# Performance work log

Measured on AMD Instinct MI355X. Metric: run time of the kernel, lower is better.

Reference implementation:

```python
import jax, jax.numpy as jnp
import numpy as np

N = 100000      # num POIs (nodes)
M = 20000       # num trajectories (hyperedges)
NNZ = 1000000   # incidence entries
D = 128         # emb_dim
NUM_LAYERS = 3
NEG_SLOPE = 0.2  # PyG HypergraphConv leaky_relu default


def setup_inputs() -> dict:
    key = jax.random.key(0)
    ks = jax.random.split(key, 8)
    pois_embs = jax.random.normal(ks[0], (N, D), jnp.float32)
    traj_embs = jax.random.normal(ks[1], (M, D), jnp.float32)
    hyperedge_weight = jax.random.uniform(ks[2], (M,), jnp.float32)
    node_idx = jax.random.randint(ks[3], (NNZ,), 0, N, jnp.int32)
    edge_idx = jax.random.randint(ks[4], (NNZ,), 0, M, jnp.int32)
    # learned params of the shared HypergraphConv layer (heads=1, concat)
    W_lin = jax.random.normal(ks[5], (D, D), jnp.float32) / np.sqrt(D).astype(np.float32)
    att = jax.random.normal(ks[6], (2 * D,), jnp.float32) * 0.1
    bias = jnp.zeros((D,), jnp.float32)
    return dict(pois_embs=pois_embs, traj_embs=traj_embs,
                hyperedge_weight=hyperedge_weight,
                node_idx=node_idx, edge_idx=edge_idx,
                W_lin=W_lin, att=att, bias=bias)


def _segment_softmax(scores, seg, num_seg):
    smax = jax.ops.segment_max(scores, seg, num_segments=num_seg)
    smax = jnp.where(jnp.isfinite(smax), smax, 0.0)  # guard empty segments
    ex = jnp.exp(scores - smax[seg])
    den = jax.ops.segment_sum(ex, seg, num_segments=num_seg)
    return ex / (den[seg] + 1e-16)


def _hconv(x, traj_embs, hyperedge_weight, node_idx, edge_idx, W_lin, att, bias):
    # x: [N, D] node feats; traj_embs: [M, D] hyperedge feats
    xt = x @ W_lin            # [N, D]  lin(x)
    et = traj_embs @ W_lin    # [M, D]  lin(hyperedge_attr)
    # attention logits per incidence pair (additive decomposition of cat*att)
    s_n = xt @ att[:D]        # [N]
    s_e = et @ att[D:]        # [M]
    alpha = jax.nn.leaky_relu(s_n[node_idx] + s_e[edge_idx], NEG_SLOPE)  # [NNZ]
    alpha = _segment_softmax(alpha, node_idx, N)  # softmax grouped by node
    # degree normalizations: D = sum_e H_ve * w_e, B = |e|
    Ddeg = jax.ops.segment_sum(hyperedge_weight[edge_idx], node_idx, num_segments=N)
    Dinv = jnp.where(Ddeg > 0, 1.0 / Ddeg, 0.0)
    Bdeg = jax.ops.segment_sum(jnp.ones((NNZ,), xt.dtype), edge_idx, num_segments=M)
    Binv = jnp.where(Bdeg > 0, 1.0 / Bdeg, 0.0)
    # node -> edge: B^{-1} H^T (alpha * x)
    msg1 = (alpha * Binv[edge_idx])[:, None] * xt[node_idx]        # [NNZ, D]
    edge_out = jax.ops.segment_sum(msg1, edge_idx, num_segments=M)  # [M, D]
    # edge -> node: D^{-1} H (alpha * edge_out)
    msg2 = (alpha * Dinv[node_idx])[:, None] * edge_out[edge_idx]   # [NNZ, D]
    out = jax.ops.segment_sum(msg2, node_idx, num_segments=N)       # [N, D]
    return out + bias


def reference(pois_embs, traj_embs, hyperedge_weight, node_idx, edge_idx, W_lin, att, bias):
    cur = pois_embs
    acc = pois_embs  # running sum of stacked layer outputs (incl. input)
    for _ in range(NUM_LAYERS):
        cur = _hconv(cur, traj_embs, hyperedge_weight, node_idx, edge_idx, W_lin, att, bias) + cur
        acc = acc + cur
    return acc / jnp.asarray(NUM_LAYERS + 1, acc.dtype)  # mean over stack
```

## Files before the change

kernel.cpp:

```cpp
#include <hip/hip_runtime.h>
#include <cstdint>
#include <cstddef>

#define DIM 128
#define NEG_SLOPE 0.2f

typedef __attribute__((ext_vector_type(8))) short short8v;
typedef __attribute__((ext_vector_type(4))) float float4v;

__device__ __forceinline__ float bf_lo(uint u) { return __uint_as_float(u << 16); }
__device__ __forceinline__ float bf_hi(uint u) { return __uint_as_float(u & 0xffff0000u); }
__device__ __forceinline__ uint f2bf(float f) {
  uint u = __float_as_uint(f);
  return (u + 0x7fffu + ((u >> 16) & 1u)) >> 16;
}
__device__ __forceinline__ uint pack_bf2(float lo, float hi) {
  return f2bf(lo) | (f2bf(hi) << 16);
}
__device__ __forceinline__ float lrelu(float x) {
  return x >= 0.0f ? x : NEG_SLOPE * x;
}

__global__ void wswz_kernel(const float* __restrict__ W, ushort* __restrict__ Wswz)
{
  int i = blockIdx.x * 256 + threadIdx.x;
  int j = i & 7, lane = (i >> 3) & 63, nt = (i >> 9) & 7, kt = i >> 12;
  int k = kt * 32 + (lane >> 4) * 8 + j;
  int col = nt * 16 + (lane & 15);
  Wswz[i] = (ushort)f2bf(W[k * 128 + col]);
}

__global__ void poisbf_kernel(const float* __restrict__ pois,
                              uint4* __restrict__ pois_bf, int N_, int NP)
{
  int i = blockIdx.x * 256 + threadIdx.x;
  if (i >= NP * 16) return;
  int row = i >> 4;
  uint4 o;
  if (row < N_) {
    const float* src = pois + (size_t)i * 8;
    float4 f0 = *(const float4*)src;
    float4 f1 = *(const float4*)(src + 4);
    o.x = pack_bf2(f0.x, f0.y); o.y = pack_bf2(f0.z, f0.w);
    o.z = pack_bf2(f1.x, f1.y); o.w = pack_bf2(f1.z, f1.w);
  } else { o.x = o.y = o.z = o.w = 0; }
  pois_bf[i] = o;
}

__global__ __launch_bounds__(256) void gemm_mfma_kernel(
    const ushort* __restrict__ Xb, const ushort* __restrict__ Wswz,
    const float* __restrict__ att, ushort* __restrict__ Yb,
    float* __restrict__ s_n, int rowsN)
{
  __shared__ ushort st[64 * 128];
  int tid = threadIdx.x;
  int w = tid >> 6, lane = tid & 63;
  int q = lane >> 4, c = lane & 15;
  int r0b = blockIdx.x * 64;
  int r0 = r0b + w * 16;
  float4v acc[8];
#pragma unroll
  for (int nt = 0; nt < 8; ++nt) acc[nt] = (float4v){0.f, 0.f, 0.f, 0.f};
  const ushort* arow = Xb + (size_t)(r0 + c) * DIM + q * 8;
#pragma unroll
  for (int kt = 0; kt < 4; ++kt) {
    short8v a = *(const short8v*)(arow + kt * 32);
#pragma unroll
    for (int nt = 0; nt < 8; ++nt) {
      short8v b = *(const short8v*)(Wswz + ((((kt << 3) + nt) << 9) + (lane << 3)));
      acc[nt] = __builtin_amdgcn_mfma_f32_16x16x32_bf16(a, b, acc[nt], 0, 0, 0);
    }
  }
  float av[8];
#pragma unroll
  for (int nt = 0; nt < 8; ++nt) av[nt] = att[nt * 16 + c];
  float p0 = 0, p1 = 0, p2 = 0, p3 = 0;
#pragma unroll
  for (int nt = 0; nt < 8; ++nt) {
    p0 = fmaf(acc[nt][0], av[nt], p0);
    p1 = fmaf(acc[nt][1], av[nt], p1);
    p2 = fmaf(acc[nt][2], av[nt], p2);
    p3 = fmaf(acc[nt][3], av[nt], p3);
  }
#pragma unroll
  for (int m = 8; m >= 1; m >>= 1) {
    p0 += __shfl_xor(p0, m, 64);
    p1 += __shfl_xor(p1, m, 64);
    p2 += __shfl_xor(p2, m, 64);
    p3 += __shfl_xor(p3, m, 64);
  }
  if (c == 0) {
    int rb = r0 + q * 4;
    if (rb + 0 < rowsN) s_n[rb + 0] = p0;
    if (rb + 1 < rowsN) s_n[rb + 1] = p1;
    if (rb + 2 < rowsN) s_n[rb + 2] = p2;
    if (rb + 3 < rowsN) s_n[rb + 3] = p3;
  }
  ushort* sw = st + w * 2048;
#pragma unroll
  for (int nt = 0; nt < 8; ++nt) {
    sw[(q * 4 + 0) * 128 + nt * 16 + c] = (ushort)f2bf(acc[nt][0]);
    sw[(q * 4 + 1) * 128 + nt * 16 + c] = (ushort)f2bf(acc[nt][1]);
    sw[(q * 4 + 2) * 128 + nt * 16 + c] = (ushort)f2bf(acc[nt][2]);
    sw[(q * 4 + 3) * 128 + nt * 16 + c] = (ushort)f2bf(acc[nt][3]);
  }
  __syncthreads();
#pragma unroll
  for (int it = 0; it < 4; ++it) {
    int idx = tid + it * 256;
    int row = idx >> 4, seg = idx & 15;
    *(uint4*)(Yb + (size_t)(r0b + row) * DIM + seg * 8) =
        *(const uint4*)&st[row * 128 + seg * 8];
  }
}

__global__ __launch_bounds__(256) void se_kernel(
    const float* __restrict__ traj, const float* __restrict__ W,
    const float* __restrict__ att, const float* __restrict__ hw,
    float* __restrict__ s_e, float2* __restrict__ se_hw, int M_)
{
  __shared__ float wv[128];
  int tid = threadIdx.x;
  if (tid < 128) {
    const float* wr = W + (size_t)tid * 128;
    float acc = 0.0f;
#pragma unroll 4
    for (int k = 0; k < 128; ++k) acc = fmaf(wr[k], att[DIM + k], acc);
    wv[tid] = acc;
  }
  __syncthreads();
  int e = blockIdx.x * 4 + (tid >> 6);
  int lane = tid & 63;
  if (e >= M_) return;
  const float* row = traj + (size_t)e * DIM;
  float v = row[lane] * wv[lane] + row[lane + 64] * wv[lane + 64];
#pragma unroll
  for (int d = 32; d > 0; d >>= 1) v += __shfl_down(v, d, 64);
  if (lane == 0) {
    s_e[e] = v;
    float2 g; g.x = v; g.y = hw[e];
    se_hw[e] = g;
  }
}

__global__ void hist_rank_kernel(const int* __restrict__ node_idx,
                                 const int* __restrict__ edge_idx,
                                 int* __restrict__ ncnt, int* __restrict__ ecnt,
                                 int* __restrict__ r_n, int* __restrict__ r_e,
                                 int nnz)
{
  int j = (blockIdx.x * blockDim.x + threadIdx.x) * 2;
  if (j >= nnz) return;
  if (j + 2 <= nnz) {
    int2 e = *(const int2*)&edge_idx[j];
    int2 n = *(const int2*)&node_idx[j];
    int a0 = atomicAdd(&ecnt[e.x], 1);
    int a1 = atomicAdd(&ecnt[e.y], 1);
    int b0 = atomicAdd(&ncnt[n.x], 1);
    int b1 = atomicAdd(&ncnt[n.y], 1);
    *(int2*)&r_e[j] = make_int2(a0, a1);
    *(int2*)&r_n[j] = make_int2(b0, b1);
  } else {
    r_e[j] = atomicAdd(&ecnt[edge_idx[j]], 1);
    r_n[j] = atomicAdd(&ncnt[node_idx[j]], 1);
  }
}

__global__ __launch_bounds__(1024) void scan_block_kernel(
    const int* __restrict__ cnt, int* __restrict__ off,
    int* __restrict__ partials, int nbins)
{
  __shared__ int ws[16];
  int tid = threadIdx.x, lane = tid & 63, wid = tid >> 6;
  int base = blockIdx.x * 4096 + tid * 4;
  int x0 = base + 0 < nbins ? cnt[base + 0] : 0;
  int x1 = base + 1 < nbins ? cnt[base + 1] : 0;
  int x2 = base + 2 < nbins ? cnt[base + 2] : 0;
  int x3 = base + 3 < nbins ? cnt[base + 3] : 0;
  int t = x0 + x1 + x2 + x3;
  int v = t;
#pragma unroll
  for (int d = 1; d < 64; d <<= 1) {
    int y = __shfl_up(v, d, 64);
    if (lane >= d) v += y;
  }
  if (lane == 63) ws[wid] = v;
  __syncthreads();
  if (tid < 16) {
    int s = ws[tid];
#pragma unroll
    for (int d = 1; d < 16; d <<= 1) {
      int y = __shfl_up(s, d, 16);
      if (tid >= d) s += y;
    }
    ws[tid] = s;
  }
  __syncthreads();
  int pre = (wid > 0 ? ws[wid - 1] : 0) + (v - t);
  if (base + 0 < nbins) off[base + 0] = pre;
  if (base + 1 < nbins) off[base + 1] = pre + x0;
  if (base + 2 < nbins) off[base + 2] = pre + x0 + x1;
  if (base + 3 < nbins) off[base + 3] = pre + x0 + x1 + x2;
  if (tid == 0) partials[blockIdx.x] = ws[15];
}

__global__ __launch_bounds__(64) void scan_partials_kernel(
    int* __restrict__ partials, int nb)
{
  int lane = threadIdx.x;
  int t = lane < nb ? partials[lane] : 0;
  int v = t;
#pragma unroll
  for (int d = 1; d < 64; d <<= 1) {
    int y = __shfl_up(v, d, 64);
    if (lane >= d) v += y;
  }
  if (lane < nb) partials[lane] = v - t;
  if (lane == 63) partials[nb] = v;
}

__global__ void add_off_kernel(int* __restrict__ off,
                               const int* __restrict__ partials,
                               int nbins, int nb)
{
  int i = blockIdx.x * blockDim.x + threadIdx.x;
  if (i < nbins) off[i] += partials[i >> 12];
  if (i == 0) off[nbins] = partials[nb];
}

__global__ void scatter_edge_kernel(const int* __restrict__ node_idx,
                                    const int* __restrict__ edge_idx,
                                    const int* __restrict__ r_e,
                                    const int* __restrict__ eoff,
                                    int* __restrict__ nd_e, int nnz)
{
  int j = (blockIdx.x * blockDim.x + threadIdx.x) * 4;
  if (j >= nnz) return;
  if (j + 4 <= nnz) {
    int4 e = *(const int4*)&edge_idx[j];
    int4 n = *(const int4*)&node_idx[j];
    int4 re = *(const int4*)&r_e[j];
    nd_e[eoff[e.x] + re.x] = n.x;
    nd_e[eoff[e.y] + re.y] = n.y;
    nd_e[eoff[e.z] + re.z] = n.z;
    nd_e[eoff[e.w] + re.w] = n.w;
  } else {
    for (int k = j; k < nnz; ++k) nd_e[eoff[edge_idx[k]] + r_e[k]] = node_idx[k];
  }
}

__global__ void scatter_node_kernel(const int* __restrict__ node_idx,
                                    const int* __restrict__ edge_idx,
                                    const int* __restrict__ r_n,
                                    const int* __restrict__ noff,
                                    int* __restrict__ eidx_n, int nnz)
{
  int j = (blockIdx.x * blockDim.x + threadIdx.x) * 4;
  if (j >= nnz) return;
  if (j + 4 <= nnz) {
    int4 e = *(const int4*)&edge_idx[j];
    int4 n = *(const int4*)&node_idx[j];
    int4 rn = *(const int4*)&r_n[j];
    eidx_n[noff[n.x] + rn.x] = e.x;
    eidx_n[noff[n.y] + rn.y] = e.y;
    eidx_n[noff[n.z] + rn.z] = e.z;
    eidx_n[noff[n.w] + rn.w] = e.w;
  } else {
    for (int k = j; k < nnz; ++k) eidx_n[noff[node_idx[k]] + r_n[k]] = edge_idx[k];
  }
}

__global__ void softstat_kernel(const int* __restrict__ noff,
                                const int* __restrict__ eidx_n,
                                const float* __restrict__ s_n,
                                const float2* __restrict__ se_hw,
                                float2* __restrict__ ns2,
                                float* __restrict__ Dinv, int N_)
{
  int n = blockIdx.x * blockDim.x + threadIdx.x;
  if (n >= N_) return;
  int s = noff[n], e1 = noff[n + 1];
  float sn = s_n[n];
  float m = -INFINITY, den = 0.0f, d = 0.0f;
  int t = s;
  for (; t + 4 <= e1; t += 4) {
    int i0 = eidx_n[t], i1 = eidx_n[t + 1], i2 = eidx_n[t + 2], i3 = eidx_n[t + 3];
    float2 g0 = se_hw[i0], g1 = se_hw[i1], g2 = se_hw[i2], g3 = se_hw[i3];
    float l0 = lrelu(sn + g0.x), l1 = lrelu(sn + g1.x);
    float l2 = lrelu(sn + g2.x), l3 = lrelu(sn + g3.x);
    float mm = fmaxf(fmaxf(fmaxf(l0, l1), fmaxf(l2, l3)), m);
    den = den * __expf(m - mm) + __expf(l0 - mm) + __expf(l1 - mm)
        + __expf(l2 - mm) + __expf(l3 - mm);
    m = mm;
    d += g0.y + g1.y + g2.y + g3.y;
  }
  for (; t < e1; ++t) {
    float2 g = se_hw[eidx_n[t]];
    float l = lrelu(sn + g.x);
    float mm = fmaxf(l, m);
    den = den * __expf(m - mm) + __expf(l - mm);
    m = mm;
    d += g.y;
  }
  if (s == e1) m = 0.0f;
  float2 r;
  r.x = sn;
  r.y = m + __logf(den + 1e-16f);
  ns2[n] = r;
  Dinv[n] = d > 0.0f ? 1.0f / d : 0.0f;
}

__global__ __launch_bounds__(256) void msg1_kernel(
    const int* __restrict__ eoff, const int* __restrict__ nd_e,
    const float2* __restrict__ ns2, const float* __restrict__ s_e,
    const ushort* __restrict__ xt, uint* __restrict__ eo, int M_)
{
  int e = blockIdx.x * (blockDim.x >> 6) + (threadIdx.x >> 6);
  int lane = threadIdx.x & 63;
  if (e >= M_) return;
  int s = eoff[e], t1 = eoff[e + 1];
  int len = t1 - s;
  float binv = len > 0 ? 1.0f / (float)len : 0.0f;
  float se = s_e[e];
  const uint* xt4 = (const uint*)xt + lane;
  float2 acc = {0.0f, 0.0f};
  int t = s;
  for (; t + 8 <= t1; t += 8) {
    int n0 = nd_e[t],     n1 = nd_e[t + 1], n2 = nd_e[t + 2], n3 = nd_e[t + 3];
    int n4 = nd_e[t + 4], n5 = nd_e[t + 5], n6 = nd_e[t + 6], n7 = nd_e[t + 7];
    float2 q0 = ns2[n0], q1 = ns2[n1], q2 = ns2[n2], q3 = ns2[n3];
    float2 q4 = ns2[n4], q5 = ns2[n5], q6 = ns2[n6], q7 = ns2[n7];
    uint u0 = xt4[(size_t)n0 * 64], u1 = xt4[(size_t)n1 * 64];
    uint u2 = xt4[(size_t)n2 * 64], u3 = xt4[(size_t)n3 * 64];
    uint u4 = xt4[(size_t)n4 * 64], u5 = xt4[(size_t)n5 * 64];
    uint u6 = xt4[(size_t)n6 * 64], u7 = xt4[(size_t)n7 * 64];
    float c0 = __expf(lrelu(q0.x + se) - q0.y);
    float c1 = __expf(lrelu(q1.x + se) - q1.y);
    float c2 = __expf(lrelu(q2.x + se) - q2.y);
    float c3 = __expf(lrelu(q3.x + se) - q3.y);
    float c4 = __expf(lrelu(q4.x + se) - q4.y);
    float c5 = __expf(lrelu(q5.x + se) - q5.y);
    float c6 = __expf(lrelu(q6.x + se) - q6.y);
    float c7 = __expf(lrelu(q7.x + se) - q7.y);
    acc.x = fmaf(c0, bf_lo(u0), acc.x); acc.y = fmaf(c0, bf_hi(u0), acc.y);
    acc.x = fmaf(c1, bf_lo(u1), acc.x); acc.y = fmaf(c1, bf_hi(u1), acc.y);
    acc.x = fmaf(c2, bf_lo(u2), acc.x); acc.y = fmaf(c2, bf_hi(u2), acc.y);
    acc.x = fmaf(c3, bf_lo(u3), acc.x); acc.y = fmaf(c3, bf_hi(u3), acc.y);
    acc.x = fmaf(c4, bf_lo(u4), acc.x); acc.y = fmaf(c4, bf_hi(u4), acc.y);
    acc.x = fmaf(c5, bf_lo(u5), acc.x); acc.y = fmaf(c5, bf_hi(u5), acc.y);
    acc.x = fmaf(c6, bf_lo(u6), acc.x); acc.y = fmaf(c6, bf_hi(u6), acc.y);
    acc.x = fmaf(c7, bf_lo(u7), acc.x); acc.y = fmaf(c7, bf_hi(u7), acc.y);
  }
  for (; t < t1; ++t) {
    int nd = nd_e[t];
    float2 q = ns2[nd];
    uint u = xt4[(size_t)nd * 64];
    float c = __expf(lrelu(q.x + se) - q.y);
    acc.x = fmaf(c, bf_lo(u), acc.x);
    acc.y = fmaf(c, bf_hi(u), acc.y);
  }
  eo[(size_t)e * (DIM / 2) + lane] = pack_bf2(acc.x * binv, acc.y * binv);
}

__global__ __launch_bounds__(256) void msg2_kernel(
    const int* __restrict__ noff, const int* __restrict__ eidx_n,
    const float2* __restrict__ ns2, const float* __restrict__ Dinv,
    const float* __restrict__ s_e, const uint* __restrict__ eo,
    const float* __restrict__ bias,
    const float* __restrict__ cur_in, const float* __restrict__ acc_in,
    float* __restrict__ cur_out, uint* __restrict__ curbf_out,
    float* __restrict__ acc_out, int last, int N_)
{
  int n = blockIdx.x * (blockDim.x >> 6) + (threadIdx.x >> 6);
  int lane = threadIdx.x & 63;
  if (n >= N_) return;
  int s = noff[n], t1 = noff[n + 1];
  float2 nsv = ns2[n];
  float sn = nsv.x, lz = nsv.y;
  const uint* eo4 = eo + lane;
  float2 acc = {0.0f, 0.0f};
  int t = s;
  for (; t + 8 <= t1; t += 8) {
    int e0 = eidx_n[t],     e1 = eidx_n[t + 1], e2 = eidx_n[t + 2], e3 = eidx_n[t + 3];
    int e4 = eidx_n[t + 4], e5 = eidx_n[t + 5], e6 = eidx_n[t + 6], e7 = eidx_n[t + 7];
    float x0 = s_e[e0], x1 = s_e[e1], x2 = s_e[e2], x3 = s_e[e3];
    float x4 = s_e[e4], x5 = s_e[e5], x6 = s_e[e6], x7 = s_e[e7];
    uint u0 = eo4[(size_t)e0 * 64], u1 = eo4[(size_t)e1 * 64];
    uint u2 = eo4[(size_t)e2 * 64], u3 = eo4[(size_t)e3 * 64];
    uint u4 = eo4[(size_t)e4 * 64], u5 = eo4[(size_t)e5 * 64];
    uint u6 = eo4[(size_t)e6 * 64], u7 = eo4[(size_t)e7 * 64];
    float c0 = __expf(lrelu(sn + x0) - lz);
    float c1 = __expf(lrelu(sn + x1) - lz);
    float c2 = __expf(lrelu(sn + x2) - lz);
    float c3 = __expf(lrelu(sn + x3) - lz);
    float c4 = __expf(lrelu(sn + x4) - lz);
    float c5 = __expf(lrelu(sn + x5) - lz);
    float c6 = __expf(lrelu(sn + x6) - lz);
    float c7 = __expf(lrelu(sn + x7) - lz);
    acc.x = fmaf(c0, bf_lo(u0), acc.x); acc.y = fmaf(c0, bf_hi(u0), acc.y);
    acc.x = fmaf(c1, bf_lo(u1), acc.x); acc.y = fmaf(c1, bf_hi(u1), acc.y);
    acc.x = fmaf(c2, bf_lo(u2), acc.x); acc.y = fmaf(c2, bf_hi(u2), acc.y);
    acc.x = fmaf(c3, bf_lo(u3), acc.x); acc.y = fmaf(c3, bf_hi(u3), acc.y);
    acc.x = fmaf(c4, bf_lo(u4), acc.x); acc.y = fmaf(c4, bf_hi(u4), acc.y);
    acc.x = fmaf(c5, bf_lo(u5), acc.x); acc.y = fmaf(c5, bf_hi(u5), acc.y);
    acc.x = fmaf(c6, bf_lo(u6), acc.x); acc.y = fmaf(c6, bf_hi(u6), acc.y);
    acc.x = fmaf(c7, bf_lo(u7), acc.x); acc.y = fmaf(c7, bf_hi(u7), acc.y);
  }
  for (; t < t1; ++t) {
    int e = eidx_n[t];
    uint u = eo4[(size_t)e * 64];
    float c = __expf(lrelu(sn + s_e[e]) - lz);
    acc.x = fmaf(c, bf_lo(u), acc.x);
    acc.y = fmaf(c, bf_hi(u), acc.y);
  }
  float sc = Dinv[n];
  float2 b = ((const float2*)bias)[lane];
  size_t idx = (size_t)n * DIM + lane * 2;
  float cx = cur_in[idx]     + acc.x * sc + b.x;
  float cy = cur_in[idx + 1] + acc.y * sc + b.y;
  if (last) {
    acc_out[idx]     = (acc_in[idx]     + cx) * 0.25f;
    acc_out[idx + 1] = (acc_in[idx + 1] + cy) * 0.25f;
  } else {
    cur_out[idx] = cx; cur_out[idx + 1] = cy;
    curbf_out[(size_t)n * 64 + lane] = pack_bf2(cx, cy);
    acc_out[idx]     = acc_in[idx]     + cx;
    acc_out[idx + 1] = acc_in[idx + 1] + cy;
  }
}

static inline int cdiv(int a, int b) { return (a + b - 1) / b; }

extern "C" void kernel_launch(void* const* d_in, const int* in_sizes, int n_in,
                              void* d_out, int out_size, void* d_ws, size_t ws_size,
                              hipStream_t stream)
{
  const float* pois = (const float*)d_in[0];
  const float* traj = (const float*)d_in[1];
  const float* hw   = (const float*)d_in[2];
  const int* node_idx = (const int*)d_in[3];
  const int* edge_idx = (const int*)d_in[4];
  const float* W    = (const float*)d_in[5];
  const float* att  = (const float*)d_in[6];
  const float* bias = (const float*)d_in[7];
  float* dout = (float*)d_out;

  const int N   = in_sizes[0] / DIM;
  const int M   = in_sizes[2];
  const int NNZ = in_sizes[3];
  const int NP  = (N + 63) & ~63;

  char* p = (char*)d_ws;
  auto alloc = [&](size_t bytes) -> void* {
    void* r = (void*)p;
    p += (bytes + 255) & ~(size_t)255;
    return r;
  };
  ushort* xt_bf   = (ushort*)alloc((size_t)NP * DIM * 2);
  ushort* cur_bf  = (ushort*)alloc((size_t)NP * DIM * 2);
  ushort* pois_bf = (ushort*)alloc((size_t)NP * DIM * 2);
  ushort* W_swz   = (ushort*)alloc(16384 * 2);
  uint*   eo_bf = (uint*)alloc((size_t)M * (DIM / 2) * 4);
  float*  cur   = (float*)alloc((size_t)N * DIM * 4);
  float2* ns2   = (float2*)alloc((size_t)N * 8);
  float*  s_e  = (float*)alloc((size_t)M * 4);
  float2* se_hw = (float2*)alloc((size_t)M * 8);
  float*  s_n  = (float*)alloc((size_t)N * 4);
  float*  Dinv = (float*)alloc((size_t)N * 4);
  int* ecnt = (int*)alloc((size_t)M * 4);
  int* ncnt = (int*)alloc((size_t)N * 4);
  int* eoff = (int*)alloc((size_t)(M + 1) * 4);
  int* noff = (int*)alloc((size_t)(N + 1) * 4);
  int* r_e  = (int*)alloc((size_t)NNZ * 4);
  int* r_n  = (int*)alloc((size_t)NNZ * 4);
  int* nd_e   = (int*)alloc((size_t)NNZ * 4);
  int* eidx_n = (int*)alloc((size_t)NNZ * 4);
  int* part_e = (int*)alloc(65 * 4);
  int* part_n = (int*)alloc(65 * 4);
  (void)ws_size;

  const int nbE = cdiv(M, 4096), nbN = cdiv(N, 4096);

  hipMemsetAsync(ecnt, 0, (size_t)M * 4, stream);
  hipMemsetAsync(ncnt, 0, (size_t)N * 4, stream);
  hist_rank_kernel<<<cdiv(NNZ, 512), 256, 0, stream>>>(node_idx, edge_idx, ncnt, ecnt, r_n, r_e, NNZ);
  scan_block_kernel<<<nbE, 1024, 0, stream>>>(ecnt, eoff, part_e, M);
  scan_block_kernel<<<nbN, 1024, 0, stream>>>(ncnt, noff, part_n, N);
  scan_partials_kernel<<<1, 64, 0, stream>>>(part_e, nbE);
  scan_partials_kernel<<<1, 64, 0, stream>>>(part_n, nbN);
  add_off_kernel<<<cdiv(M, 256), 256, 0, stream>>>(eoff, part_e, M, nbE);
  add_off_kernel<<<cdiv(N, 256), 256, 0, stream>>>(noff, part_n, N, nbN);
  scatter_edge_kernel<<<cdiv(NNZ, 1024), 256, 0, stream>>>(node_idx, edge_idx, r_e, eoff, nd_e, NNZ);
  scatter_node_kernel<<<cdiv(NNZ, 1024), 256, 0, stream>>>(node_idx, edge_idx, r_n, noff, eidx_n, NNZ);

  wswz_kernel<<<64, 256, 0, stream>>>(W, W_swz);
  se_kernel<<<cdiv(M, 4), 256, 0, stream>>>(traj, W, att, hw, s_e, se_hw, M);
  poisbf_kernel<<<cdiv(NP * 16, 256), 256, 0, stream>>>(pois, (uint4*)pois_bf, N, NP);

  for (int layer = 0; layer < 3; ++layer) {
    const ushort* gin = (layer == 0) ? pois_bf : cur_bf;
    gemm_mfma_kernel<<<NP / 64, 256, 0, stream>>>(gin, W_swz, att, xt_bf, s_n, N);
    softstat_kernel<<<cdiv(N, 256), 256, 0, stream>>>(noff, eidx_n, s_n, se_hw, ns2, Dinv, N);
    msg1_kernel<<<cdiv(M, 4), 256, 0, stream>>>(eoff, nd_e, ns2, s_e, xt_bf, eo_bf, M);
    const float* cin = (layer == 0) ? pois : cur;
    const float* ain = (layer == 0) ? pois : dout;
    int last = (layer == 2) ? 1 : 0;
    msg2_kernel<<<cdiv(N, 4), 256, 0, stream>>>(noff, eidx_n, ns2, Dinv, s_e, eo_bf,
                                                bias, cin, ain, cur, (uint*)cur_bf,
                                                dout, last, N);
  }
}
```

Measured before the change: 742.9 us.

## Replicate histogram counters to reduce atomic contention in CSR build

The incidence histogram is split across several replicated counter arrays (16 for edges, 8 for nodes), with each thread picking a replica by thread index to spread atomics. A new per-bin pass turns the replica counts into exclusive prefixes and totals, and the offset kernel adds the global offset into every replica so the scatter kernels can find each entry's slot. This costs larger memsets, extra passes over the replica arrays, and more scattered reads in the scatter step, in exchange for fewer same-address atomic collisions.

```diff
diff --git a/kernel.cpp b/kernel.cpp
--- a/kernel.cpp
+++ b/kernel.cpp
@@ -4,6 +4,9 @@
 
 #define DIM 128
 #define NEG_SLOPE 0.2f
+
+#define EREP 16
+#define NREP 8
 
 typedef __attribute__((ext_vector_type(8))) short short8v;
 typedef __attribute__((ext_vector_type(4))) float float4v;
@@ -145,25 +148,43 @@
 
 __global__ void hist_rank_kernel(const int* __restrict__ node_idx,
                                  const int* __restrict__ edge_idx,
-                                 int* __restrict__ ncnt, int* __restrict__ ecnt,
+                                 int* __restrict__ ncnt_r, int* __restrict__ ecnt_r,
                                  int* __restrict__ r_n, int* __restrict__ r_e,
-                                 int nnz)
-{
-  int j = (blockIdx.x * blockDim.x + threadIdx.x) * 2;
+                                 int nnz, int M_, int N_)
+{
+  int t = blockIdx.x * blockDim.x + threadIdx.x;
+  int j = t * 2;
   if (j >= nnz) return;
+  int* ec = ecnt_r + (size_t)(t & (EREP - 1)) * M_;
+  int* nc = ncnt_r + (size_t)(t & (NREP - 1)) * N_;
   if (j + 2 <= nnz) {
     int2 e = *(const int2*)&edge_idx[j];
     int2 n = *(const int2*)&node_idx[j];
-    int a0 = atomicAdd(&ecnt[e.x], 1);
-    int a1 = atomicAdd(&ecnt[e.y], 1);
-    int b0 = atomicAdd(&ncnt[n.x], 1);
-    int b1 = atomicAdd(&ncnt[n.y], 1);
+    int a0 = atomicAdd(&ec[e.x], 1);
+    int a1 = atomicAdd(&ec[e.y], 1);
+    int b0 = atomicAdd(&nc[n.x], 1);
+    int b1 = atomicAdd(&nc[n.y], 1);
     *(int2*)&r_e[j] = make_int2(a0, a1);
     *(int2*)&r_n[j] = make_int2(b0, b1);
   } else {
-    r_e[j] = atomicAdd(&ecnt[edge_idx[j]], 1);
-    r_n[j] = atomicAdd(&ncnt[node_idx[j]], 1);
-  }
+    r_e[j] = atomicAdd(&ec[edge_idx[j]], 1);
+    r_n[j] = atomicAdd(&nc[node_idx[j]], 1);
+  }
+}
+
+__global__ void repsum_kernel(int* __restrict__ cnt_r, int* __restrict__ cnt,
+                              int nbins, int reps)
+{
+  int b = blockIdx.x * blockDim.x + threadIdx.x;
+  if (b >= nbins) return;
+  int s = 0;
+  for (int r = 0; r < reps; ++r) {
+    size_t o = (size_t)r * nbins + b;
+    int v = cnt_r[o];
+    cnt_r[o] = s;
+    s += v;
+  }
+  cnt[b] = s;
 }
 
 __global__ __launch_bounds__(1024) void scan_block_kernel(
@@ -219,54 +240,69 @@
   if (lane == 63) partials[nb] = v;
 }
 
-__global__ void add_off_kernel(int* __restrict__ off,
-                               const int* __restrict__ partials,
-                               int nbins, int nb)
+__global__ void add_off_combine_kernel(int* __restrict__ off,
+                                       const int* __restrict__ partials,
+                                       int* __restrict__ pre,
+                                       int nbins, int nb, int reps)
 {
   int i = blockIdx.x * blockDim.x + threadIdx.x;
-  if (i < nbins) off[i] += partials[i >> 12];
+  if (i < nbins) {
+    int o = off[i] + partials[i >> 12];
+    off[i] = o;
+    for (int r = 0; r < reps; ++r) pre[(size_t)r * nbins + i] += o;
+  }
   if (i == 0) off[nbins] = partials[nb];
 }
 
 __global__ void scatter_edge_kernel(const int* __restrict__ node_idx,
                                     const int* __restrict__ edge_idx,
                                     const int* __restrict__ r_e,
-                                    const int* __restrict__ eoff,
-                                    int* __restrict__ nd_e, int nnz)
+                                    const int* __restrict__ pre_e,
+                                    int* __restrict__ nd_e, int nnz, int M_)
 {
   int j = (blockIdx.x * blockDim.x + threadIdx.x) * 4;
   if (j >= nnz) return;
   if (j + 4 <= nnz) {
+    const int* p0 = pre_e + (size_t)((j >> 1) & (EREP - 1)) * M_;
+    const int* p1 = pre_e + (size_t)(((j >> 1) + 1) & (EREP - 1)) * M_;
     int4 e = *(const int4*)&edge_idx[j];
     int4 n = *(const int4*)&node_idx[j];
     int4 re = *(const int4*)&r_e[j];
-    nd_e[eoff[e.x] + re.x] = n.x;
-    nd_e[eoff[e.y] + re.y] = n.y;
-    nd_e[eoff[e.z] + re.z] = n.z;
-    nd_e[eoff[e.w] + re.w] = n.w;
+    nd_e[p0[e.x] + re.x] = n.x;
+    nd_e[p0[e.y] + re.y] = n.y;
+    nd_e[p1[e.z] + re.z] = n.z;
+    nd_e[p1[e.w] + re.w] = n.w;
   } else {
-    for (int k = j; k < nnz; ++k) nd_e[eoff[edge_idx[k]] + r_e[k]] = node_idx[k];
+    for (int k = j; k < nnz; ++k) {
+      const int* pp = pre_e + (size_t)((k >> 1) & (EREP - 1)) * M_;
+      nd_e[pp[edge_idx[k]] + r_e[k]] = node_idx[k];
+    }
   }
 }
 
 __global__ void scatter_node_kernel(const int* __restrict__ node_idx,
                                     const int* __restrict__ edge_idx,
                                     const int* __restrict__ r_n,
-                                    const int* __restrict__ noff,
-                                    int* __restrict__ eidx_n, int nnz)
+                                    const int* __restrict__ pre_n,
+                                    int* __restrict__ eidx_n, int nnz, int N_)
 {
   int j = (blockIdx.x * blockDim.x + threadIdx.x) * 4;
   if (j >= nnz) return;
   if (j + 4 <= nnz) {
+    const int* p0 = pre_n + (size_t)((j >> 1) & (NREP - 1)) * N_;
+    const int* p1 = pre_n + (size_t)(((j >> 1) + 1) & (NREP - 1)) * N_;
     int4 e = *(const int4*)&edge_idx[j];
     int4 n = *(const int4*)&node_idx[j];
     int4 rn = *(const int4*)&r_n[j];
-    eidx_n[noff[n.x] + rn.x] = e.x;
-    eidx_n[noff[n.y] + rn.y] = e.y;
-    eidx_n[noff[n.z] + rn.z] = e.z;
-    eidx_n[noff[n.w] + rn.w] = e.w;
+    eidx_n[p0[n.x] + rn.x] = e.x;
+    eidx_n[p0[n.y] + rn.y] = e.y;
+    eidx_n[p1[n.z] + rn.z] = e.z;
+    eidx_n[p1[n.w] + rn.w] = e.w;
   } else {
-    for (int k = j; k < nnz; ++k) eidx_n[noff[node_idx[k]] + r_n[k]] = edge_idx[k];
+    for (int k = j; k < nnz; ++k) {
+      const int* pp = pre_n + (size_t)((k >> 1) & (NREP - 1)) * N_;
+      eidx_n[pp[node_idx[k]] + r_n[k]] = edge_idx[k];
+    }
   }
 }
 
@@ -467,8 +503,10 @@
   float2* se_hw = (float2*)alloc((size_t)M * 8);
   float*  s_n  = (float*)alloc((size_t)N * 4);
   float*  Dinv = (float*)alloc((size_t)N * 4);
-  int* ecnt = (int*)alloc((size_t)M * 4);
-  int* ncnt = (int*)alloc((size_t)N * 4);
+  int* ecnt   = (int*)alloc((size_t)M * 4);
+  int* ncnt   = (int*)alloc((size_t)N * 4);
+  int* ecnt_r = (int*)alloc((size_t)EREP * M * 4);
+  int* ncnt_r = (int*)alloc((size_t)NREP * N * 4);
   int* eoff = (int*)alloc((size_t)(M + 1) * 4);
   int* noff = (int*)alloc((size_t)(N + 1) * 4);
   int* r_e  = (int*)alloc((size_t)NNZ * 4);
@@ -481,17 +519,19 @@
 
   const int nbE = cdiv(M, 4096), nbN = cdiv(N, 4096);
 
-  hipMemsetAsync(ecnt, 0, (size_t)M * 4, stream);
-  hipMemsetAsync(ncnt, 0, (size_t)N * 4, stream);
-  hist_rank_kernel<<<cdiv(NNZ, 512), 256, 0, stream>>>(node_idx, edge_idx, ncnt, ecnt, r_n, r_e, NNZ);
+  hipMemsetAsync(ecnt_r, 0, (size_t)EREP * M * 4, stream);
+  hipMemsetAsync(ncnt_r, 0, (size_t)NREP * N * 4, stream);
+  hist_rank_kernel<<<cdiv(NNZ, 512), 256, 0, stream>>>(node_idx, edge_idx, ncnt_r, ecnt_r, r_n, r_e, NNZ, M, N);
+  repsum_kernel<<<cdiv(M, 256), 256, 0, stream>>>(ecnt_r, ecnt, M, EREP);
+  repsum_kernel<<<cdiv(N, 256), 256, 0, stream>>>(ncnt_r, ncnt, N, NREP);
   scan_block_kernel<<<nbE, 1024, 0, stream>>>(ecnt, eoff, part_e, M);
   scan_block_kernel<<<nbN, 1024, 0, stream>>>(ncnt, noff, part_n, N);
   scan_partials_kernel<<<1, 64, 0, stream>>>(part_e, nbE);
   scan_partials_kernel<<<1, 64, 0, stream>>>(part_n, nbN);
-  add_off_kernel<<<cdiv(M, 256), 256, 0, stream>>>(eoff, part_e, M, nbE);
-  add_off_kernel<<<cdiv(N, 256), 256, 0, stream>>>(noff, part_n, N, nbN);
-  scatter_edge_kernel<<<cdiv(NNZ, 1024), 256, 0, stream>>>(node_idx, edge_idx, r_e, eoff, nd_e, NNZ);
-  scatter_node_kernel<<<cdiv(NNZ, 1024), 256, 0, stream>>>(node_idx, edge_idx, r_n, noff, eidx_n, NNZ);
+  add_off_combine_kernel<<<cdiv(M, 256), 256, 0, stream>>>(eoff, part_e, ecnt_r, M, nbE, EREP);
+  add_off_combine_kernel<<<cdiv(N, 256), 256, 0, stream>>>(noff, part_n, ncnt_r, N, nbN, NREP);
+  scatter_edge_kernel<<<cdiv(NNZ, 1024), 256, 0, stream>>>(node_idx, edge_idx, r_e, ecnt_r, nd_e, NNZ, M);
+  scatter_node_kernel<<<cdiv(NNZ, 1024), 256, 0, stream>>>(node_idx, edge_idx, r_n, ncnt_r, eidx_n, NNZ, N);
 
   wswz_kernel<<<64, 256, 0, stream>>>(W, W_swz);
   se_kernel<<<cdiv(M, 4), 256, 0, stream>>>(traj, W, att, hw, s_e, se_hw, M);
```

After: 754.9 us. No clear change (+1.6%).
